# Kernel tuning notes

Hardware: AMD Instinct MI355X
Metric: run time of the kernel (lower is better)

The kernel has to match this reference:

```python
import jax, jax.numpy as jnp
import numpy as np

B, F_IN, T_IN = 256, 3, 800
C, K, H, N_OUT = 128, 15, 150, 10

def hard_sigmoid(x):
    # Keras-style hard sigmoid used by LSTMHardSigmoid: clamp(0.2*x + 0.5, 0, 1)
    return jnp.clip(0.2 * x + 0.5, 0.0, 1.0)

def setup_inputs() -> dict:
    key = jax.random.key(0)
    ks = jax.random.split(key, 16)
    mk = lambda k, s, sc=0.05: (jax.random.normal(k, s, dtype=jnp.float32) * sc)
    return {
        "x": jax.random.normal(ks[0], (B, F_IN, T_IN), dtype=jnp.float32),
        "conv_w": mk(ks[1], (C, F_IN, K), 0.1),
        "conv_b": jnp.zeros((C,), jnp.float32),
        # PyTorch LSTM layout: [4H, in] with gate order i,f,g,o
        "w_ih_f": mk(ks[2], (4 * H, C)),
        "w_hh_f": mk(ks[3], (4 * H, H)),
        "b_ih_f": mk(ks[4], (4 * H,)),
        "b_hh_f": mk(ks[5], (4 * H,)),
        "w_ih_b": mk(ks[6], (4 * H, C)),
        "w_hh_b": mk(ks[7], (4 * H, H)),
        "b_ih_b": mk(ks[8], (4 * H,)),
        "b_hh_b": mk(ks[9], (4 * H,)),
        "lin1_w": mk(ks[10], (50, 2 * H)),
        "lin1_b": jnp.zeros((50,), jnp.float32),
        "lin2_w": mk(ks[11], (N_OUT, 50)),
        "lin2_b": jnp.zeros((N_OUT,), jnp.float32),
    }

def _lstm_dir(xseq, w_ih, w_hh, b_ih, b_hh, reverse):
    # xseq: [B, T, C] -> pre-activations [B, T, 4H]
    pre = jnp.einsum('btc,gc->btg', xseq, w_ih) + b_ih + b_hh
    pre_t = jnp.swapaxes(pre, 0, 1)  # [T, B, 4H]
    h0 = jnp.zeros((xseq.shape[0], H), pre.dtype)
    c0 = jnp.zeros((xseq.shape[0], H), pre.dtype)
    def step(carry, gt):
        h, c = carry
        g = gt + h @ w_hh.T
        i, f, gg, o = jnp.split(g, 4, axis=-1)
        c = hard_sigmoid(f) * c + hard_sigmoid(i) * jnp.tanh(gg)
        h = hard_sigmoid(o) * jnp.tanh(c)
        return (h, c), h
    _, hs = jax.lax.scan(step, (h0, c0), pre_t, reverse=reverse)
    return jnp.swapaxes(hs, 0, 1)  # [B, T, H]

def reference(x, conv_w, conv_b, w_ih_f, w_hh_f, b_ih_f, b_hh_f,
              w_ih_b, w_hh_b, b_ih_b, b_hh_b, lin1_w, lin1_b, lin2_w, lin2_b):
    # net1: Conv1d (VALID) + ReLU + (Dropout: identity at eval) + MaxPool1d(2)
    y = jax.lax.conv_general_dilated(
        x, conv_w, window_strides=(1,), padding='VALID',
        dimension_numbers=('NCH', 'OIH', 'NCH')) + conv_b[None, :, None]
    y = jax.nn.relu(y)                       # [B, 128, 786]
    L = y.shape[2] // 2
    y = y[:, :, :2 * L].reshape(y.shape[0], y.shape[1], L, 2).max(axis=-1)  # [B,128,393]
    xseq = jnp.transpose(y, (0, 2, 1))       # [B, 393, 128]
    # net2: bidirectional LSTM with hard-sigmoid gates
    h_fwd = _lstm_dir(xseq, w_ih_f, w_hh_f, b_ih_f, b_hh_f, reverse=False)
    h_bwd = _lstm_dir(xseq, w_ih_b, w_hh_b, b_ih_b, b_hh_b, reverse=True)
    bi = jnp.concatenate([h_fwd, h_bwd], axis=-1)  # [B, T, 300]
    # global max-pool over time (F.max_pool1d with kernel = full length)
    pooled = bi.max(axis=1)                  # [B, 300]
    # net3: Linear + ReLU + (Dropout identity) + Linear + Softmax(dim=1)
    z = jax.nn.relu(pooled @ lin1_w.T + lin1_b)
    logits = z @ lin2_w.T + lin2_b
    return jax.nn.softmax(logits, axis=1)
```

## Files before the change

kernel.cpp:

```cpp
#include <hip/hip_runtime.h>
#include <cstdio>

#define BATCH 256
#define TSEQ  393
#define CH    128
#define FIN   3
#define TIN   800
#define KK    15
#define HID   150
#define NPAD  640
#define KPAD  160
#define NB    16
#define HALF_A 197
#define HALF_B 196
#define SLOTSTRIDE (16*10240)

typedef _Float16 half_t;
typedef __attribute__((ext_vector_type(8))) _Float16 h8v;
typedef __attribute__((ext_vector_type(4))) _Float16 h4v;
typedef __attribute__((ext_vector_type(4))) float f4v;

__device__ inline float hsig(float x){ return fminf(fmaxf(fmaf(0.2f, x, 0.5f), 0.f), 1.f); }
__device__ inline float tanh_(float x){
  float e = __expf(2.f*x);
  return fmaf(-2.f, __builtin_amdgcn_rcpf(e + 1.f), 1.f);
}

#define DPPF(v, ctrl) __int_as_float(__builtin_amdgcn_mov_dpp(__float_as_int(v), ctrl, 0xF, 0xF, true))
#define XPOSE_PAIR(va, vb, om, CTRL) { float t_ = om ? va : vb; t_ = DPPF(t_, CTRL); va = om ? t_ : va; vb = om ? vb : t_; }

__global__ void prep_wih(const float* __restrict__ wf, const float* __restrict__ wb,
                         half_t* __restrict__ out){
  int i = blockIdx.x*256 + threadIdx.x;
  if (i >= 2*NPAD*CH) return;
  int c = i & 127; int n = (i >> 7) % NPAD; int d = i / (NPAD*CH);
  const float* src = d ? wb : wf;
  float v = 0.f;
  if (n < 600){ int j = n >> 2, g = n & 3; v = src[(g*HID + j)*CH + c]; }
  out[i] = (half_t)v;
}
__global__ void prep_whh(const float* __restrict__ wf, const float* __restrict__ wb,
                         half_t* __restrict__ out){
  int i = blockIdx.x*256 + threadIdx.x;
  if (i >= 2*NPAD*KPAD) return;
  int kc = i % KPAD; int n = (i / KPAD) % NPAD; int d = i / (NPAD*KPAD);
  const float* src = d ? wb : wf;
  float v = 0.f;
  if (n < 600 && kc < HID){ int j = n >> 2, g = n & 3; v = src[(g*HID + j)*HID + kc]; }
  out[i] = (half_t)v;
}
__global__ void prep_bsum(const float* __restrict__ bihf, const float* __restrict__ bhhf,
                          const float* __restrict__ bihb, const float* __restrict__ bhhb,
                          float* __restrict__ out){
  int i = blockIdx.x*256 + threadIdx.x;
  if (i >= 2*NPAD) return;
  int n = i % NPAD; int d = i / NPAD;
  float v = 0.f;
  if (n < 600){ int j = n >> 2, g = n & 3; int r = g*HID + j;
    v = d ? (bihb[r] + bhhb[r]) : (bihf[r] + bhhf[r]); }
  out[i] = v;
}

#define CTT 32
__global__ __launch_bounds__(256) void conv_pool(const float* __restrict__ x,
                                                 const float* __restrict__ w,
                                                 const float* __restrict__ bias,
                                                 half_t* __restrict__ xseq){
  __shared__ float wl[CH*FIN*KK];
  __shared__ float xl[FIN][2*CTT + 14];
  int tid = threadIdx.x;
  int b = blockIdx.x, t0 = blockIdx.y*CTT;
  for (int i = tid; i < CH*FIN*KK; i += 256) wl[i] = w[i];
  int p0 = 2*t0;
  for (int i = tid; i < FIN*(2*CTT+14); i += 256){
    int f = i/(2*CTT+14), q = i%(2*CTT+14);
    int p = p0 + q;
    xl[f][q] = (p < TIN) ? x[((size_t)b*FIN + f)*TIN + p] : 0.f;
  }
  __syncthreads();
  int c = tid & 127, th = tid >> 7;
  float a0[16], a1[16];
  #pragma unroll
  for (int i=0;i<16;++i){ a0[i]=0.f; a1[i]=0.f; }
  #pragma unroll
  for (int f=0; f<FIN; ++f){
    float xv[46];
    #pragma unroll
    for (int q=0;q<46;++q) xv[q] = xl[f][th*32 + q];
    #pragma unroll
    for (int k=0;k<KK;++k){
      float ws = wl[c*FIN*KK + f*KK + k];
      #pragma unroll
      for (int i=0;i<16;++i){
        a0[i] = fmaf(xv[2*i+k],   ws, a0[i]);
        a1[i] = fmaf(xv[2*i+k+1], ws, a1[i]);
      }
    }
  }
  float bc = bias[c];
  #pragma unroll
  for (int i=0;i<16;++i){
    int t = t0 + th*16 + i;
    if (t < TSEQ){
      float v = fmaxf(fmaxf(a0[i], a1[i]) + bc, 0.f);
      xseq[((size_t)b*TSEQ + t)*CH + c] = (half_t)v;
    }
  }
}

__global__ __launch_bounds__(512) void proj(const half_t* __restrict__ xseq,
                                            const half_t* __restrict__ wih,
                                            const float* __restrict__ bsum,
                                            half_t* __restrict__ pre,
                                            int off){
  int bt4 = blockIdx.x;
  int s   = blockIdx.y;
  int d   = blockIdx.z;
  int sg  = s + off;
  int t   = d ? (TSEQ-1 - sg) : sg;
  int tid = threadIdx.x, wv = tid >> 6, ln = tid & 63;
  int m = ln & 15, kg = ln >> 4;

  h8v bfr[5][4]; float bs[5];
  #pragma unroll
  for (int i = 0; i < 5; ++i){
    int n = (wv*5 + i)*16 + m;
    #pragma unroll
    for (int ks = 0; ks < 4; ++ks)
      bfr[i][ks] = *(const h8v*)(wih + ((size_t)d*NPAD + n)*CH + ks*32 + kg*8);
    bs[i] = bsum[d*NPAD + n];
  }
  #pragma unroll
  for (int ms = 0; ms < 4; ++ms){
    int b = bt4*64 + ms*16 + m;
    h8v ax[4];
    #pragma unroll
    for (int ks = 0; ks < 4; ++ks)
      ax[ks] = *(const h8v*)(xseq + ((size_t)b*TSEQ + t)*CH + ks*32 + kg*8);
    #pragma unroll
    for (int i = 0; i < 5; ++i){
      f4v acc = {bs[i], bs[i], bs[i], bs[i]};
      #pragma unroll
      for (int ks = 0; ks < 4; ++ks)
        acc = __builtin_amdgcn_mfma_f32_16x16x32_f16(ax[ks], bfr[i][ks], acc, 0, 0, 0);
      int n = (wv*5 + i)*16 + m;
      h4v hv = {(half_t)acc[0], (half_t)acc[1], (half_t)acc[2], (half_t)acc[3]};
      *(h4v*)(pre + (((size_t)d*HALF_A + s)*16 + (bt4*4 + ms))*10240 + n*16 + kg*4) = hv;
    }
  }
}

__global__ __launch_bounds__(512, 2) void recur(const half_t* __restrict__ pre,
                                                const half_t* __restrict__ whh,
                                                float* __restrict__ pooled,
                                                float* __restrict__ stateC,
                                                half_t* __restrict__ stateH,
                                                int first, int last, int nsteps){
  __shared__ __align__(16) half_t hbuf[2*NB*168];

  int tid = threadIdx.x, wv = tid >> 6, ln = tid & 63;
  int m = ln & 15, kg = ln >> 4;
  int bt = blockIdx.x, d = blockIdx.y;
  int b0 = bt*NB;
  int blk = d*16 + bt;
  bool o1 = (ln & 1), o2 = (ln & 2);

  h8v bhh[5][5];
  #pragma unroll
  for (int i = 0; i < 5; ++i){
    int n = (wv*5 + i)*16 + m;
    #pragma unroll
    for (int ks = 0; ks < 5; ++ks)
      bhh[i][ks] = *(const h8v*)(whh + ((size_t)d*NPAD + n)*KPAD + ks*32 + kg*8);
  }
  #pragma unroll
  for (int i = 0; i < 5; ++i)
    #pragma unroll
    for (int ks = 0; ks < 5; ++ks)
      asm volatile("" : "+v"(bhh[i][ks]));

  int jc[5], bc_;
  bc_ = kg*4 + (m&3);
  #pragma unroll
  for (int T = 0; T < 5; ++T) jc[T] = 20*wv + 4*T + (m>>2);

  float c_reg[5], hm_reg[5];
  if (first){
    for (int i = tid; i < NB*168; i += 512) hbuf[i] = (half_t)0.f;
    for (int i = tid; i < NB*168; i += 512) hbuf[NB*168 + i] = (half_t)0.f;
    #pragma unroll
    for (int T = 0; T < 5; ++T){ c_reg[T] = 0.f; hm_reg[T] = -1e30f; }
  } else {
    for (int i = tid; i < NB*168; i += 512) hbuf[i] = stateH[(size_t)blk*NB*168 + i];
    for (int i = tid; i < NB*168; i += 512) hbuf[NB*168 + i] = (half_t)0.f;
    const float* sc = stateC + ((size_t)blk*512 + tid)*10;
    #pragma unroll
    for (int T = 0; T < 5; ++T){ c_reg[T] = sc[T]; hm_reg[T] = sc[5+T]; }
  }
  __syncthreads();

  const half_t* psrc = pre + ((size_t)d*HALF_A*16 + bt)*10240;
  int pofl = wv*1280 + m*16 + kg*4;

  h4v curp[5];
  #pragma unroll
  for (int T = 0; T < 5; ++T) curp[T] = *(const h4v*)(psrc + pofl + T*256);

  int p = 0;
  #pragma unroll 1
  for (int s = 0; s < nsteps; ++s){
    const half_t* nsrc = psrc + ((s+1 < nsteps) ? SLOTSTRIDE : 0);
    h4v nxt[5];
    #pragma unroll
    for (int T = 0; T < 5; ++T) nxt[T] = *(const h4v*)(nsrc + pofl + T*256);

    const half_t* hrd = hbuf + p*NB*168 + m*168;
    h8v ah[5];
    #pragma unroll
    for (int ks = 0; ks < 5; ++ks) ah[ks] = *(const h8v*)(hrd + ks*32 + kg*8);

    f4v acc[5];
    #pragma unroll
    for (int T = 0; T < 5; ++T){
      f4v a = {0.f, 0.f, 0.f, 0.f};
      #pragma unroll
      for (int ks = 0; ks < 5; ++ks)
        a = __builtin_amdgcn_mfma_f32_16x16x32_f16(ah[ks], bhh[T][ks], a, 0, 0, 0);
      acc[T] = a;
    }

    half_t* hwr = hbuf + (p^1)*NB*168 + bc_*168;
    #pragma unroll
    for (int T = 0; T < 5; ++T){
      float v0 = acc[T][0] + (float)curp[T][0];
      float v1 = acc[T][1] + (float)curp[T][1];
      float v2 = acc[T][2] + (float)curp[T][2];
      float v3 = acc[T][3] + (float)curp[T][3];
      XPOSE_PAIR(v0, v1, o1, 0xB1);
      XPOSE_PAIR(v2, v3, o1, 0xB1);
      XPOSE_PAIR(v0, v2, o2, 0x4E);
      XPOSE_PAIR(v1, v3, o2, 0x4E);
      float cn = hsig(v1)*c_reg[T] + hsig(v0)*tanh_(v2);
      float hn = hsig(v3)*tanh_(cn);
      c_reg[T] = cn;
      hm_reg[T] = fmaxf(hm_reg[T], hn);
      hwr[jc[T]] = (half_t)hn;
    }

    #pragma unroll
    for (int T = 0; T < 5; ++T) curp[T] = nxt[T];

    asm volatile("s_waitcnt lgkmcnt(0)" ::: "memory");
    __builtin_amdgcn_s_barrier();
    __builtin_amdgcn_sched_barrier(0);
    p ^= 1;
    psrc += SLOTSTRIDE;
  }

  if (!last){
    for (int i = tid; i < NB*168; i += 512) stateH[(size_t)blk*NB*168 + i] = hbuf[p*NB*168 + i];
    float* sc = stateC + ((size_t)blk*512 + tid)*10;
    #pragma unroll
    for (int T = 0; T < 5; ++T){ sc[T] = c_reg[T]; sc[5+T] = hm_reg[T]; }
  } else {
    #pragma unroll
    for (int T = 0; T < 5; ++T){
      if (jc[T] < HID) pooled[(size_t)(b0 + bc_)*300 + d*HID + jc[T]] = hm_reg[T];
    }
  }
}

__global__ __launch_bounds__(256) void fc(const float* __restrict__ pooled,
                                          const float* __restrict__ w1, const float* __restrict__ b1,
                                          const float* __restrict__ w2, const float* __restrict__ b2,
                                          float* __restrict__ out){
  __shared__ float prow[300];
  __shared__ float ps[64][5];
  __shared__ float z[52];
  __shared__ float lg[12];
  int b = blockIdx.x, tid = threadIdx.x;
  for (int i = tid; i < 300; i += 256) prow[i] = pooled[(size_t)b*300 + i];
  __syncthreads();
  int j = tid & 63, seg = tid >> 6;
  float a = 0.f;
  if (j < 50){
    const float* wr = w1 + (size_t)j*300 + seg*75;
    const float* pr = prow + seg*75;
    #pragma unroll 5
    for (int k = 0; k < 75; ++k) a = fmaf(pr[k], wr[k], a);
  }
  ps[j][seg] = a;
  __syncthreads();
  if (tid < 50) z[tid] = fmaxf(ps[tid][0]+ps[tid][1]+ps[tid][2]+ps[tid][3] + b1[tid], 0.f);
  __syncthreads();
  if (tid < 10){
    float a2 = b2[tid];
    for (int k = 0; k < 50; ++k) a2 = fmaf(z[k], w2[tid*50 + k], a2);
    lg[tid] = a2;
  }
  __syncthreads();
  if (tid < 10){
    float mx = lg[0];
    #pragma unroll
    for (int k = 1; k < 10; ++k) mx = fmaxf(mx, lg[k]);
    float ssum = 0.f;
    #pragma unroll
    for (int k = 0; k < 10; ++k) ssum += __expf(lg[k] - mx);
    out[(size_t)b*10 + tid] = __expf(lg[tid] - mx) / ssum;
  }
}

extern "C" void kernel_launch(void* const* d_in, const int* in_sizes, int n_in,
                              void* d_out, int out_size, void* d_ws, size_t ws_size,
                              hipStream_t stream) {
  const float* x      = (const float*)d_in[0];
  const float* conv_w = (const float*)d_in[1];
  const float* conv_b = (const float*)d_in[2];
  const float* w_ih_f = (const float*)d_in[3];
  const float* w_hh_f = (const float*)d_in[4];
  const float* b_ih_f = (const float*)d_in[5];
  const float* b_hh_f = (const float*)d_in[6];
  const float* w_ih_b = (const float*)d_in[7];
  const float* w_hh_b = (const float*)d_in[8];
  const float* b_ih_b = (const float*)d_in[9];
  const float* b_hh_b = (const float*)d_in[10];
  const float* l1w = (const float*)d_in[11];
  const float* l1b = (const float*)d_in[12];
  const float* l2w = (const float*)d_in[13];
  const float* l2b = (const float*)d_in[14];
  float* out = (float*)d_out;

  char* ws = (char*)d_ws;
  size_t off = 0;
  auto alloc = [&](size_t bytes){ size_t o = off; off += (bytes + 255) & ~(size_t)255; return o; };
  size_t xseq_o = alloc((size_t)BATCH*TSEQ*CH*2);
  size_t pre_o  = alloc((size_t)2*HALF_A*16*10240*2);
  size_t wih_o  = alloc((size_t)2*NPAD*CH*2);
  size_t whh_o  = alloc((size_t)2*NPAD*KPAD*2);
  size_t bs_o   = alloc((size_t)2*NPAD*4);
  size_t pool_o = alloc((size_t)BATCH*300*4);
  size_t stc_o  = alloc((size_t)32*512*10*4);
  size_t sth_o  = alloc((size_t)32*NB*168*2);
  if (off > ws_size){
    fprintf(stderr, "[cnnblstm] WS TOO SMALL: need %zu have %zu\n", off, ws_size);
    return;
  }
  half_t* xseq_p = (half_t*)(ws + xseq_o);
  half_t* pre_p  = (half_t*)(ws + pre_o);
  half_t* wih_p  = (half_t*)(ws + wih_o);
  half_t* whh_p  = (half_t*)(ws + whh_o);
  float*  bs_p   = (float*)(ws + bs_o);
  float*  pool_p = (float*)(ws + pool_o);
  float*  stc_p  = (float*)(ws + stc_o);
  half_t* sth_p  = (half_t*)(ws + sth_o);

  prep_wih <<<(2*NPAD*CH + 255)/256, 256, 0, stream>>>(w_ih_f, w_ih_b, wih_p);
  prep_whh <<<(2*NPAD*KPAD + 255)/256, 256, 0, stream>>>(w_hh_f, w_hh_b, whh_p);
  prep_bsum<<<(2*NPAD + 255)/256, 256, 0, stream>>>(b_ih_f, b_hh_f, b_ih_b, b_hh_b, bs_p);
  conv_pool<<<dim3(BATCH, (TSEQ + CTT - 1)/CTT), 256, 0, stream>>>(x, conv_w, conv_b, xseq_p);

  proj <<<dim3(4, HALF_A, 2), 512, 0, stream>>>(xseq_p, wih_p, bs_p, pre_p, 0);
  recur<<<dim3(16, 2), 512, 0, stream>>>(pre_p, whh_p, pool_p, stc_p, sth_p, 1, 0, HALF_A);
  proj <<<dim3(4, HALF_B, 2), 512, 0, stream>>>(xseq_p, wih_p, bs_p, pre_p, HALF_A);
  recur<<<dim3(16, 2), 512, 0, stream>>>(pre_p, whh_p, pool_p, stc_p, sth_p, 0, 1, HALF_B);

  fc<<<BATCH, 256, 0, stream>>>(pool_p, l1w, l1b, l2w, l2b, out);
}
```

Measured before the change: 666.7 us.

## Pin recurrent weights in AGPRs, hand-schedule MFMAs, prefetch pre-activations two steps ahead

Recurrent weight fragments now live in accumulation registers (AGPRs) through asm constraints, which frees VGPRs. The 25 MFMAs per step are written as interleaved inline assembly, so the five independent accumulators alternate and dependent MFMAs are not issued back to back. Pre-activation loads are double-buffered two steps ahead instead of one, to hide global-load latency in the serial recurrence. The risks are hand-placed s_nop hazard padding that may not suit this chip, and the compiler losing freedom to schedule around the asm blocks.

```diff
diff --git a/kernel.cpp b/kernel.cpp
--- a/kernel.cpp
+++ b/kernel.cpp
@@ -165,19 +165,17 @@
   int blk = d*16 + bt;
   bool o1 = (ln & 1), o2 = (ln & 2);
 
-  h8v bhh[5][5];
+  h8v bA[5][5];
   #pragma unroll
   for (int i = 0; i < 5; ++i){
     int n = (wv*5 + i)*16 + m;
     #pragma unroll
-    for (int ks = 0; ks < 5; ++ks)
-      bhh[i][ks] = *(const h8v*)(whh + ((size_t)d*NPAD + n)*KPAD + ks*32 + kg*8);
-  }
-  #pragma unroll
-  for (int i = 0; i < 5; ++i)
-    #pragma unroll
-    for (int ks = 0; ks < 5; ++ks)
-      asm volatile("" : "+v"(bhh[i][ks]));
+    for (int ks = 0; ks < 5; ++ks){
+      h8v w = *(const h8v*)(whh + ((size_t)d*NPAD + n)*KPAD + ks*32 + kg*8);
+      asm volatile("" : "+a"(w));
+      bA[i][ks] = w;
+    }
+  }
 
   int jc[5], bc_;
   bc_ = kg*4 + (m&3);
@@ -199,35 +197,84 @@
   }
   __syncthreads();
 
-  const half_t* psrc = pre + ((size_t)d*HALF_A*16 + bt)*10240;
+  const half_t* pb = pre + ((size_t)d*HALF_A*16 + bt)*10240;
   int pofl = wv*1280 + m*16 + kg*4;
 
-  h4v curp[5];
-  #pragma unroll
-  for (int T = 0; T < 5; ++T) curp[T] = *(const h4v*)(psrc + pofl + T*256);
+  h4v curp[5], nA[5];
+  #pragma unroll
+  for (int T = 0; T < 5; ++T) curp[T] = *(const h4v*)(pb + pofl + T*256);
+  {
+    const half_t* p1 = pb + (size_t)(nsteps > 1 ? 1 : 0)*SLOTSTRIDE;
+    #pragma unroll
+    for (int T = 0; T < 5; ++T) nA[T] = *(const h4v*)(p1 + pofl + T*256);
+  }
 
   int p = 0;
   #pragma unroll 1
   for (int s = 0; s < nsteps; ++s){
-    const half_t* nsrc = psrc + ((s+1 < nsteps) ? SLOTSTRIDE : 0);
-    h4v nxt[5];
-    #pragma unroll
-    for (int T = 0; T < 5; ++T) nxt[T] = *(const h4v*)(nsrc + pofl + T*256);
+    int s2 = (s+2 < nsteps) ? s+2 : nsteps-1;
+    const half_t* p2 = pb + (size_t)s2*SLOTSTRIDE;
+    h4v nB[5];
+    #pragma unroll
+    for (int T = 0; T < 5; ++T) nB[T] = *(const h4v*)(p2 + pofl + T*256);
 
     const half_t* hrd = hbuf + p*NB*168 + m*168;
-    h8v ah[5];
-    #pragma unroll
-    for (int ks = 0; ks < 5; ++ks) ah[ks] = *(const h8v*)(hrd + ks*32 + kg*8);
+    h8v ah0 = *(const h8v*)(hrd + 0*32 + kg*8);
+    h8v ah1 = *(const h8v*)(hrd + 1*32 + kg*8);
+    h8v ah2 = *(const h8v*)(hrd + 2*32 + kg*8);
+    h8v ah3 = *(const h8v*)(hrd + 3*32 + kg*8);
+    h8v ah4 = *(const h8v*)(hrd + 4*32 + kg*8);
 
     f4v acc[5];
     #pragma unroll
-    for (int T = 0; T < 5; ++T){
-      f4v a = {0.f, 0.f, 0.f, 0.f};
-      #pragma unroll
-      for (int ks = 0; ks < 5; ++ks)
-        a = __builtin_amdgcn_mfma_f32_16x16x32_f16(ah[ks], bhh[T][ks], a, 0, 0, 0);
-      acc[T] = a;
-    }
+    for (int T = 0; T < 5; ++T) acc[T] = (f4v){0.f, 0.f, 0.f, 0.f};
+
+    asm volatile(
+      "s_nop 1\n\t"
+      "v_mfma_f32_16x16x32_f16 %0, %5, %7, %0\n\t"
+      "v_mfma_f32_16x16x32_f16 %1, %5, %9, %1\n\t"
+      "v_mfma_f32_16x16x32_f16 %2, %5, %11, %2\n\t"
+      "v_mfma_f32_16x16x32_f16 %3, %5, %13, %3\n\t"
+      "v_mfma_f32_16x16x32_f16 %4, %5, %15, %4\n\t"
+      "v_mfma_f32_16x16x32_f16 %0, %6, %8, %0\n\t"
+      "v_mfma_f32_16x16x32_f16 %1, %6, %10, %1\n\t"
+      "v_mfma_f32_16x16x32_f16 %2, %6, %12, %2\n\t"
+      "v_mfma_f32_16x16x32_f16 %3, %6, %14, %3\n\t"
+      "v_mfma_f32_16x16x32_f16 %4, %6, %16, %4"
+      : "+v"(acc[0]), "+v"(acc[1]), "+v"(acc[2]), "+v"(acc[3]), "+v"(acc[4])
+      : "v"(ah0), "v"(ah1),
+        "a"(bA[0][0]), "a"(bA[0][1]),
+        "a"(bA[1][0]), "a"(bA[1][1]),
+        "a"(bA[2][0]), "a"(bA[2][1]),
+        "a"(bA[3][0]), "a"(bA[3][1]),
+        "a"(bA[4][0]), "a"(bA[4][1]));
+    __builtin_amdgcn_sched_barrier(0);
+    asm volatile(
+      "v_mfma_f32_16x16x32_f16 %0, %5, %8, %0\n\t"
+      "v_mfma_f32_16x16x32_f16 %1, %5, %11, %1\n\t"
+      "v_mfma_f32_16x16x32_f16 %2, %5, %14, %2\n\t"
+      "v_mfma_f32_16x16x32_f16 %3, %5, %17, %3\n\t"
+      "v_mfma_f32_16x16x32_f16 %4, %5, %20, %4\n\t"
+      "v_mfma_f32_16x16x32_f16 %0, %6, %9, %0\n\t"
+      "v_mfma_f32_16x16x32_f16 %1, %6, %12, %1\n\t"
+      "v_mfma_f32_16x16x32_f16 %2, %6, %15, %2\n\t"
+      "v_mfma_f32_16x16x32_f16 %3, %6, %18, %3\n\t"
+      "v_mfma_f32_16x16x32_f16 %4, %6, %21, %4\n\t"
+      "v_mfma_f32_16x16x32_f16 %0, %7, %10, %0\n\t"
+      "v_mfma_f32_16x16x32_f16 %1, %7, %13, %1\n\t"
+      "v_mfma_f32_16x16x32_f16 %2, %7, %16, %2\n\t"
+      "v_mfma_f32_16x16x32_f16 %3, %7, %19, %3\n\t"
+      "v_mfma_f32_16x16x32_f16 %4, %7, %22, %4\n\t"
+      "s_nop 7\n\t"
+      "s_nop 7"
+      : "+v"(acc[0]), "+v"(acc[1]), "+v"(acc[2]), "+v"(acc[3]), "+v"(acc[4])
+      : "v"(ah2), "v"(ah3), "v"(ah4),
+        "a"(bA[0][2]), "a"(bA[0][3]), "a"(bA[0][4]),
+        "a"(bA[1][2]), "a"(bA[1][3]), "a"(bA[1][4]),
+        "a"(bA[2][2]), "a"(bA[2][3]), "a"(bA[2][4]),
+        "a"(bA[3][2]), "a"(bA[3][3]), "a"(bA[3][4]),
+        "a"(bA[4][2]), "a"(bA[4][3]), "a"(bA[4][4]));
+    __builtin_amdgcn_sched_barrier(0);
 
     half_t* hwr = hbuf + (p^1)*NB*168 + bc_*168;
     #pragma unroll
@@ -248,13 +295,14 @@
     }
 
     #pragma unroll
-    for (int T = 0; T < 5; ++T) curp[T] = nxt[T];
+    for (int T = 0; T < 5; ++T) curp[T] = nA[T];
+    #pragma unroll
+    for (int T = 0; T < 5; ++T) nA[T] = nB[T];
 
     asm volatile("s_waitcnt lgkmcnt(0)" ::: "memory");
     __builtin_amdgcn_s_barrier();
     __builtin_amdgcn_sched_barrier(0);
     p ^= 1;
-    psrc += SLOTSTRIDE;
   }
 
   if (!last){
```

Result: slower. 731.7 us (+9.7%).

## Pin recurrent weights in AGPRs, interleave MFMA chains, prefetch two steps ahead

Applied to the files above, without the earlier changes.

Loads the W_hh fragments straight into fixed accumulation registers (a0-a99) with inline asm, so the 5x5 MFMA inner product reads its B operand from AGPRs. That frees VGPRs under the 2-waves-per-SIMD launch bound. The MFMAs are reordered so the five independent accumulator chains interleave, which hides MFMA dependency latency, and an explicit s_nop pair is added before the results are read. The pre-activation prefetch now runs two timesteps ahead instead of one, to cover global load latency on the serial recurrence. The hand-written asm and register clobbers are brittle and depend on the compiler not otherwise using those AGPRs.

```diff
diff --git a/kernel.cpp b/kernel.cpp
--- a/kernel.cpp
+++ b/kernel.cpp
@@ -150,6 +150,32 @@
   }
 }
 
+#define PIN4(R0,R1,R2,R3, V) asm volatile( \
+  "v_accvgpr_write_b32 " R0 ", %0\n\t" \
+  "v_accvgpr_write_b32 " R1 ", %1\n\t" \
+  "v_accvgpr_write_b32 " R2 ", %2\n\t" \
+  "v_accvgpr_write_b32 " R3 ", %3" \
+  :: "v"(V[0]), "v"(V[1]), "v"(V[2]), "v"(V[3]) : R0, R1, R2, R3)
+
+#define LP(I,KS, R0,R1,R2,R3) { \
+  h8v w_ = *(const h8v*)(whh + ((size_t)d*NPAD + ((wv*5+(I))*16+m))*KPAD + (KS)*32 + kg*8); \
+  f4v wf_; __builtin_memcpy(&wf_, &w_, 16); \
+  PIN4(R0,R1,R2,R3, wf_); }
+
+#define MF0(ACC, AH, AR) asm volatile("v_mfma_f32_16x16x32_f16 %0, %1, " AR ", 0"  : "=v"(ACC) : "v"(AH))
+#define MF(ACC, AH, AR)  asm volatile("v_mfma_f32_16x16x32_f16 %0, %1, " AR ", %0" : "+v"(ACC) : "v"(AH))
+
+#define ACLOBS "a0","a1","a2","a3","a4","a5","a6","a7","a8","a9",\
+"a10","a11","a12","a13","a14","a15","a16","a17","a18","a19",\
+"a20","a21","a22","a23","a24","a25","a26","a27","a28","a29",\
+"a30","a31","a32","a33","a34","a35","a36","a37","a38","a39",\
+"a40","a41","a42","a43","a44","a45","a46","a47","a48","a49",\
+"a50","a51","a52","a53","a54","a55","a56","a57","a58","a59",\
+"a60","a61","a62","a63","a64","a65","a66","a67","a68","a69",\
+"a70","a71","a72","a73","a74","a75","a76","a77","a78","a79",\
+"a80","a81","a82","a83","a84","a85","a86","a87","a88","a89",\
+"a90","a91","a92","a93","a94","a95","a96","a97","a98","a99"
+
 __global__ __launch_bounds__(512, 2) void recur(const half_t* __restrict__ pre,
                                                 const half_t* __restrict__ whh,
                                                 float* __restrict__ pooled,
@@ -165,19 +191,16 @@
   int blk = d*16 + bt;
   bool o1 = (ln & 1), o2 = (ln & 2);
 
-  h8v bhh[5][5];
-  #pragma unroll
-  for (int i = 0; i < 5; ++i){
-    int n = (wv*5 + i)*16 + m;
-    #pragma unroll
-    for (int ks = 0; ks < 5; ++ks)
-      bhh[i][ks] = *(const h8v*)(whh + ((size_t)d*NPAD + n)*KPAD + ks*32 + kg*8);
-  }
-  #pragma unroll
-  for (int i = 0; i < 5; ++i)
-    #pragma unroll
-    for (int ks = 0; ks < 5; ++ks)
-      asm volatile("" : "+v"(bhh[i][ks]));
+  LP(0,0,"a0","a1","a2","a3")    LP(0,1,"a4","a5","a6","a7")    LP(0,2,"a8","a9","a10","a11")
+  LP(0,3,"a12","a13","a14","a15") LP(0,4,"a16","a17","a18","a19")
+  LP(1,0,"a20","a21","a22","a23") LP(1,1,"a24","a25","a26","a27") LP(1,2,"a28","a29","a30","a31")
+  LP(1,3,"a32","a33","a34","a35") LP(1,4,"a36","a37","a38","a39")
+  LP(2,0,"a40","a41","a42","a43") LP(2,1,"a44","a45","a46","a47") LP(2,2,"a48","a49","a50","a51")
+  LP(2,3,"a52","a53","a54","a55") LP(2,4,"a56","a57","a58","a59")
+  LP(3,0,"a60","a61","a62","a63") LP(3,1,"a64","a65","a66","a67") LP(3,2,"a68","a69","a70","a71")
+  LP(3,3,"a72","a73","a74","a75") LP(3,4,"a76","a77","a78","a79")
+  LP(4,0,"a80","a81","a82","a83") LP(4,1,"a84","a85","a86","a87") LP(4,2,"a88","a89","a90","a91")
+  LP(4,3,"a92","a93","a94","a95") LP(4,4,"a96","a97","a98","a99")
 
   int jc[5], bc_;
   bc_ = kg*4 + (m&3);
@@ -199,36 +222,49 @@
   }
   __syncthreads();
 
-  const half_t* psrc = pre + ((size_t)d*HALF_A*16 + bt)*10240;
+  const half_t* pb = pre + ((size_t)d*HALF_A*16 + bt)*10240;
   int pofl = wv*1280 + m*16 + kg*4;
 
-  h4v curp[5];
-  #pragma unroll
-  for (int T = 0; T < 5; ++T) curp[T] = *(const h4v*)(psrc + pofl + T*256);
+  h4v curp[5], nA[5];
+  #pragma unroll
+  for (int T = 0; T < 5; ++T) curp[T] = *(const h4v*)(pb + pofl + T*256);
+  {
+    const half_t* p1 = pb + (size_t)(nsteps > 1 ? 1 : 0)*SLOTSTRIDE;
+    #pragma unroll
+    for (int T = 0; T < 5; ++T) nA[T] = *(const h4v*)(p1 + pofl + T*256);
+  }
 
   int p = 0;
   #pragma unroll 1
   for (int s = 0; s < nsteps; ++s){
-    const half_t* nsrc = psrc + ((s+1 < nsteps) ? SLOTSTRIDE : 0);
-    h4v nxt[5];
-    #pragma unroll
-    for (int T = 0; T < 5; ++T) nxt[T] = *(const h4v*)(nsrc + pofl + T*256);
+    int s2 = (s+2 < nsteps) ? s+2 : nsteps-1;
+    const half_t* p2 = pb + (size_t)s2*SLOTSTRIDE;
+    h4v nB[5];
+    #pragma unroll
+    for (int T = 0; T < 5; ++T) nB[T] = *(const h4v*)(p2 + pofl + T*256);
 
     const half_t* hrd = hbuf + p*NB*168 + m*168;
-    h8v ah[5];
-    #pragma unroll
-    for (int ks = 0; ks < 5; ++ks) ah[ks] = *(const h8v*)(hrd + ks*32 + kg*8);
-
-    f4v acc[5];
-    #pragma unroll
-    for (int T = 0; T < 5; ++T){
-      f4v a = {0.f, 0.f, 0.f, 0.f};
-      #pragma unroll
-      for (int ks = 0; ks < 5; ++ks)
-        a = __builtin_amdgcn_mfma_f32_16x16x32_f16(ah[ks], bhh[T][ks], a, 0, 0, 0);
-      acc[T] = a;
-    }
-
+    h8v ah0 = *(const h8v*)(hrd + 0*32 + kg*8);
+    h8v ah1 = *(const h8v*)(hrd + 1*32 + kg*8);
+    h8v ah2 = *(const h8v*)(hrd + 2*32 + kg*8);
+    h8v ah3 = *(const h8v*)(hrd + 3*32 + kg*8);
+    h8v ah4 = *(const h8v*)(hrd + 4*32 + kg*8);
+
+    f4v acc0, acc1, acc2, acc3, acc4;
+    MF0(acc0, ah0, "a[0:3]");   MF0(acc1, ah0, "a[20:23]"); MF0(acc2, ah0, "a[40:43]");
+    MF0(acc3, ah0, "a[60:63]"); MF0(acc4, ah0, "a[80:83]");
+    MF (acc0, ah1, "a[4:7]");   MF (acc1, ah1, "a[24:27]"); MF (acc2, ah1, "a[44:47]");
+    MF (acc3, ah1, "a[64:67]"); MF (acc4, ah1, "a[84:87]");
+    MF (acc0, ah2, "a[8:11]");  MF (acc1, ah2, "a[28:31]"); MF (acc2, ah2, "a[48:51]");
+    MF (acc3, ah2, "a[68:71]"); MF (acc4, ah2, "a[88:91]");
+    MF (acc0, ah3, "a[12:15]"); MF (acc1, ah3, "a[32:35]"); MF (acc2, ah3, "a[52:55]");
+    MF (acc3, ah3, "a[72:75]"); MF (acc4, ah3, "a[92:95]");
+    MF (acc0, ah4, "a[16:19]"); MF (acc1, ah4, "a[36:39]"); MF (acc2, ah4, "a[56:59]");
+    MF (acc3, ah4, "a[76:79]"); MF (acc4, ah4, "a[96:99]");
+    asm volatile("s_nop 7\n\ts_nop 7"
+                 : "+v"(acc0), "+v"(acc1), "+v"(acc2), "+v"(acc3), "+v"(acc4));
+
+    f4v acc[5] = {acc0, acc1, acc2, acc3, acc4};
     half_t* hwr = hbuf + (p^1)*NB*168 + bc_*168;
     #pragma unroll
     for (int T = 0; T < 5; ++T){
@@ -248,13 +284,14 @@
     }
 
     #pragma unroll
-    for (int T = 0; T < 5; ++T) curp[T] = nxt[T];
-
-    asm volatile("s_waitcnt lgkmcnt(0)" ::: "memory");
+    for (int T = 0; T < 5; ++T) curp[T] = nA[T];
+    #pragma unroll
+    for (int T = 0; T < 5; ++T) nA[T] = nB[T];
+
+    asm volatile("s_waitcnt lgkmcnt(0)" ::: "memory", ACLOBS);
     __builtin_amdgcn_s_barrier();
     __builtin_amdgcn_sched_barrier(0);
     p ^= 1;
-    psrc += SLOTSTRIDE;
   }
 
   if (!last){
```

Measured after the change: 714.4 us. 7.2% more time.
